# Kernel tuning notes

Hardware: AMD Instinct MI355X
Metric: run time of the kernel (lower is better)

## Reference

```python
import jax, jax.numpy as jnp
from jax import lax
import numpy as np

B, T, CIN, COUT = 64, 16384, 8, 8
N_A, N_B = 3, 3


def setup_inputs() -> dict:
    key = jax.random.key(0)
    k1, k2, k3, k4 = jax.random.split(key, 4)
    u = jax.random.normal(k1, (B, T, CIN), dtype=jnp.float32)
    x0 = jax.random.normal(k2, (B, N_A, COUT), dtype=jnp.float32)
    # Small AR coefficients so the IIR recursion is stable (sum |a_k| < 1).
    a_coeff = jax.random.uniform(k3, (N_A, COUT), dtype=jnp.float32,
                                 minval=-0.15, maxval=0.15)
    b_coeff = jax.random.normal(k4, (N_B + 1, CIN, COUT), dtype=jnp.float32)
    return {"u": u, "x0": x0, "a_coeff": a_coeff, "b_coeff": b_coeff}


def reference(u, x0, a_coeff, b_coeff):
    n_b = b_coeff.shape[0] - 1
    n_a = a_coeff.shape[0]
    # Causal FIR part: pad front of time axis, valid conv, channels_last.
    u_pad = jnp.pad(u, ((0, 0), (n_b, 0), (0, 0)))
    b_u = lax.conv_general_dilated(
        u_pad, b_coeff, window_strides=(1,), padding='VALID',
        dimension_numbers=('NWC', 'WIO', 'NWC'))  # [B, T, COUT]
    if n_a == 0:
        return b_u
    # Fold initial condition x0 into the first time step.
    first = b_u[:, 0, :] + jnp.einsum('to,bto->bo', jnp.flip(a_coeff, axis=0), x0)
    b_u = jnp.concatenate([first[:, None, :], b_u[:, 1:, :]], axis=1)
    # Stack n_a shifted copies (prepend tail of x0): [B, n_a, T, COUT]
    stacked = jnp.stack(
        [jnp.concatenate([x0[:, n_a - idx:, :], b_u[:, idx:, :]], axis=1)
         for idx in range(n_a)], axis=1)
    # Companion-style transition: a_ss[s, n, o] = a_coeff[n, o] if n >= s else 0.
    a_ss = jnp.stack(
        [jnp.pad(a_coeff[idx:, :], ((idx, 0), (0, 0))) for idx in range(n_a)],
        axis=0)  # [n_a, n_a, COUT]

    def a_apply(x, y):
        return jnp.einsum('sno,bnto->bsto', a_ss, x) + y

    y = lax.associative_scan(a_apply, stacked, axis=2)
    return y[:, 0, :, :]  # [B, T, COUT]
```

## Files before the change

kernel.cpp:

```cpp
#include <hip/hip_runtime.h>

#define T_SZ   16384
#define CIN    8
#define COUT   8
#define NPART  16
#define PART_T 1024
#define NCHUNK 32
#define CHT    32
#define GRID_BLOCKS (64 * NPART)
#define BAR_OFFSET_BYTES (1 << 17)

struct V3 { float x, y, z; };
__device__ __forceinline__ V3 mkv3(float a, float b, float c) { V3 r; r.x=a; r.y=b; r.z=c; return r; }
__device__ __forceinline__ V3 vadd3(V3 a, V3 b) { return mkv3(a.x+b.x, a.y+b.y, a.z+b.z); }
__device__ __forceinline__ V3 vfma3(V3 acc, float s, V3 w) {
  return mkv3(fmaf(s, w.x, acc.x), fmaf(s, w.y, acc.y), fmaf(s, w.z, acc.z));
}
__device__ __forceinline__ V3 aappf(float a0, float a1, float a2, V3 v) {
  float t2 = a2 * v.z;
  float t1 = fmaf(a1, v.y, t2);
  return mkv3(fmaf(a0, v.x, t1), t1, t2);
}
__device__ __forceinline__ V3 comb(float a0, float a1, float a2, V3 l, V3 r) {
  return vadd3(aappf(a0, a1, a2, l), r);
}

struct Row { float4 lo, hi; };
__device__ __forceinline__ Row ldrow(const float* p) {
  Row r; r.lo = *(const float4*)p; r.hi = *(const float4*)(p + 4); return r;
}
__device__ __forceinline__ Row zrow() { Row r; r.lo = make_float4(0.f,0.f,0.f,0.f); r.hi = r.lo; return r; }
__device__ __forceinline__ float rdot(const Row& r, const float* w) {
  float s = r.lo.x * w[0];
  s = fmaf(r.lo.y, w[1], s); s = fmaf(r.lo.z, w[2], s); s = fmaf(r.lo.w, w[3], s);
  s = fmaf(r.hi.x, w[4], s); s = fmaf(r.hi.y, w[5], s); s = fmaf(r.hi.z, w[6], s);
  s = fmaf(r.hi.w, w[7], s);
  return s;
}

struct Pre {
  float bv[CHT];
  V3 e0, e1, E5;
  float a0, a1, a2;
  int o, c, p, b, t0;
};

__device__ __forceinline__ void preamble(
    Pre& P, const float* __restrict__ u, const float* __restrict__ x0,
    const float* __restrict__ ac, const float* __restrict__ bc)
{
  const int j = threadIdx.x;
  P.o = j & 7;  P.c = j >> 3;
  P.p = blockIdx.x & 15;  P.b = blockIdx.x >> 4;
  const int o = P.o;
  P.a0 = ac[0*COUT + o];  P.a1 = ac[1*COUT + o];  P.a2 = ac[2*COUT + o];
  const float a0 = P.a0, a1 = P.a1, a2 = P.a2;

  float w0[8], w1[8], w2[8], w3[8];
#pragma unroll
  for (int i = 0; i < 8; ++i) {
    w0[i] = bc[(0*CIN + i)*COUT + o];
    w1[i] = bc[(1*CIN + i)*COUT + o];
    w2[i] = bc[(2*CIN + i)*COUT + o];
    w3[i] = bc[(3*CIN + i)*COUT + o];
  }

  const float* ub = u + (size_t)P.b * T_SZ * CIN;
  P.t0 = P.p * PART_T + P.c * CHT;
  const int t0 = P.t0;

  {
    Row ra, rb, rc;
    if (t0 == 0) { ra = zrow(); rb = zrow(); rc = zrow(); }
    else {
      ra = ldrow(ub + (size_t)(t0 - 3) * CIN);
      rb = ldrow(ub + (size_t)(t0 - 2) * CIN);
      rc = ldrow(ub + (size_t)(t0 - 1) * CIN);
    }
#pragma unroll
    for (int r = 0; r < CHT; ++r) {
      Row rd = ldrow(ub + (size_t)(t0 + r) * CIN);
      P.bv[r] = rdot(ra, w0) + rdot(rb, w1) + rdot(rc, w2) + rdot(rd, w3);
      ra = rb; rb = rc; rc = rd;
    }
  }

  P.e0 = mkv3(0,0,0);  P.e1 = mkv3(0,0,0);
  if (t0 == 0) {
    float x00 = x0[((size_t)P.b*3 + 0)*COUT + o];
    float x01 = x0[((size_t)P.b*3 + 1)*COUT + o];
    float x02 = x0[((size_t)P.b*3 + 2)*COUT + o];
    float first = P.bv[0] + a2*x00 + a1*x01 + a0*x02;
    P.e0 = mkv3(first, x02, x01);
    P.e1 = mkv3(P.bv[1], P.bv[1], x02);
  }

  V3 gt[6];
  gt[0] = mkv3(1.f,1.f,1.f);
#pragma unroll
  for (int k = 1; k <= 5; ++k) gt[k] = aappf(a0,a1,a2, gt[k-1]);
  V3 acc;
  if (t0 == 0) {
    V3 q0 = P.e0, q1 = P.e1;
#pragma unroll
    for (int k = 0; k < 5; ++k) q0 = aappf(a0,a1,a2, q0);
#pragma unroll
    for (int k = 0; k < 4; ++k) q1 = aappf(a0,a1,a2, q1);
    acc = vadd3(q0, q1);
#pragma unroll
    for (int r = 2; r < CHT; ++r) acc = vfma3(acc, P.bv[r], gt[5 - __popc(r)]);
  } else {
    acc = mkv3(0,0,0);
#pragma unroll
    for (int r = 0; r < CHT; ++r) acc = vfma3(acc, P.bv[r], gt[5 - __popc(r)]);
  }
  P.E5 = acc;
}

__global__ __launch_bounds__(256) void ldtf_p1(
    const float* __restrict__ u, const float* __restrict__ x0,
    const float* __restrict__ ac, const float* __restrict__ bc,
    float* __restrict__ ws)
{
  __shared__ V3 s_E5[NCHUNK*8];
  __shared__ V3 s_tr[30*8];

  Pre P;
  preamble(P, u, x0, ac, bc);
  const int j = threadIdx.x, o = P.o;
  const float a0 = P.a0, a1 = P.a1, a2 = P.a2;

  s_E5[P.c*8 + o] = P.E5;
  __syncthreads();
  if (j < 128) { int i = j >> 3; s_tr[i*8+o]      = comb(a0,a1,a2, s_E5[(2*i)*8+o],    s_E5[(2*i+1)*8+o]); }
  __syncthreads();
  if (j < 64)  { int i = j >> 3; s_tr[(16+i)*8+o] = comb(a0,a1,a2, s_tr[(2*i)*8+o],    s_tr[(2*i+1)*8+o]); }
  __syncthreads();
  if (j < 32)  { int i = j >> 3; s_tr[(24+i)*8+o] = comb(a0,a1,a2, s_tr[(16+2*i)*8+o], s_tr[(16+2*i+1)*8+o]); }
  __syncthreads();
  if (j < 16)  { int i = j >> 3; s_tr[(28+i)*8+o] = comb(a0,a1,a2, s_tr[(24+2*i)*8+o], s_tr[(24+2*i+1)*8+o]); }
  __syncthreads();
  if (j < 8) {
    V3 rt = comb(a0,a1,a2, s_tr[28*8+o], s_tr[29*8+o]);
    float* wp = ws + ((size_t)(P.b*NPART + P.p)*8 + o)*3;
    wp[0] = rt.x; wp[1] = rt.y; wp[2] = rt.z;
  }
}

#define POOL_FLOATS 8448

__global__ __launch_bounds__(256) void ldtf_p2(
    const float* __restrict__ u, const float* __restrict__ x0,
    const float* __restrict__ ac, const float* __restrict__ bc,
    float* __restrict__ out, const float* __restrict__ ws)
{
  __shared__ __align__(16) float s_pool[POOL_FLOATS];
  V3* s_E5 = (V3*)s_pool;
  V3* s_tr = (V3*)s_pool + 256;
  V3* s_mt = (V3*)s_pool + 496;
  float* s_out = s_pool;

  Pre P;
  preamble(P, u, x0, ac, bc);
  const int j = threadIdx.x, o = P.o, c = P.c, p = P.p, b = P.b;
  const float a0 = P.a0, a1 = P.a1, a2 = P.a2;

  s_E5[c*8 + o] = P.E5;
  if (j < 128) {
    int c2 = j >> 3;
    const float* wp = ws + ((size_t)(b*NPART + c2)*8 + o)*3;
    s_mt[c2*8+o] = mkv3(wp[0], wp[1], wp[2]);
  }
  __syncthreads();

  if (j < 128) { int i = j >> 3; s_tr[i*8+o]      = comb(a0,a1,a2, s_E5[(2*i)*8+o],    s_E5[(2*i+1)*8+o]); }
  else         { int i = (j-128) >> 3; if (i < 8) s_mt[(16+i)*8+o] = comb(a0,a1,a2, s_mt[(2*i)*8+o], s_mt[(2*i+1)*8+o]); }
  __syncthreads();
  if (j < 64)  { int i = j >> 3; s_tr[(16+i)*8+o] = comb(a0,a1,a2, s_tr[(2*i)*8+o],    s_tr[(2*i+1)*8+o]); }
  else if (j >= 128) { int i = (j-128) >> 3; if (i < 4) s_mt[(24+i)*8+o] = comb(a0,a1,a2, s_mt[(16+2*i)*8+o], s_mt[(16+2*i+1)*8+o]); }
  __syncthreads();
  if (j < 32)  { int i = j >> 3; s_tr[(24+i)*8+o] = comb(a0,a1,a2, s_tr[(16+2*i)*8+o], s_tr[(16+2*i+1)*8+o]); }
  else if (j >= 128) { int i = (j-128) >> 3; if (i < 2) s_mt[(28+i)*8+o] = comb(a0,a1,a2, s_mt[(24+2*i)*8+o], s_mt[(24+2*i+1)*8+o]); }
  __syncthreads();
  if (j < 16)  { int i = j >> 3; s_tr[(28+i)*8+o] = comb(a0,a1,a2, s_tr[(24+2*i)*8+o], s_tr[(24+2*i+1)*8+o]); }
  __syncthreads();

  V3 sig = mkv3(0,0,0);
  if ((p >> 3) & 1) sig = comb(a0,a1,a2, sig, s_mt[(28 + (p>>3) - 1)*8 + o]);
  if ((p >> 2) & 1) sig = comb(a0,a1,a2, sig, s_mt[(24 + (p>>2) - 1)*8 + o]);
  if ((p >> 1) & 1) sig = comb(a0,a1,a2, sig, s_mt[(16 + (p>>1) - 1)*8 + o]);
  if (p & 1)        sig = comb(a0,a1,a2, sig, s_mt[(p - 1)*8 + o]);
  if ((c >> 4) & 1) sig = comb(a0,a1,a2, sig, s_tr[(28 + (c>>4) - 1)*8 + o]);
  if ((c >> 3) & 1) sig = comb(a0,a1,a2, sig, s_tr[(24 + (c>>3) - 1)*8 + o]);
  if ((c >> 2) & 1) sig = comb(a0,a1,a2, sig, s_tr[(16 + (c>>2) - 1)*8 + o]);
  if ((c >> 1) & 1) sig = comb(a0,a1,a2, sig, s_tr[((c>>1) - 1)*8 + o]);
  if (c & 1)        sig = comb(a0,a1,a2, sig, s_E5[(c - 1)*8 + o]);

  V3 tau;
  {
    int q = p + 1;
    if (q == 16) tau = comb(a0,a1,a2, s_mt[28*8+o], s_mt[29*8+o]);
    else {
      tau = mkv3(0,0,0);
      if ((q >> 3) & 1) tau = comb(a0,a1,a2, tau, s_mt[(28 + (q>>3) - 1)*8 + o]);
      if ((q >> 2) & 1) tau = comb(a0,a1,a2, tau, s_mt[(24 + (q>>2) - 1)*8 + o]);
      if ((q >> 1) & 1) tau = comb(a0,a1,a2, tau, s_mt[(16 + (q>>1) - 1)*8 + o]);
      if (q & 1)        tau = comb(a0,a1,a2, tau, s_mt[(q - 1)*8 + o]);
    }
  }
  __syncthreads();

  if (c >= 1) s_out[(c - 1)*264 + 31*8 + o] = sig.x;
  if (c == NCHUNK - 1) s_out[31*264 + 31*8 + o] = tau.x;

  {
    V3 st[5];
#pragma unroll
    for (int r = 0; r < CHT - 1; ++r) {
      V3 v = mkv3(P.bv[r], P.bv[r], P.bv[r]);
      if (P.t0 == 0) { if (r == 0) v = P.e0; if (r == 1) v = P.e1; }
      if (r & 1)          v = comb(a0,a1,a2, st[0], v);
      if ((r & 3) == 3)   v = comb(a0,a1,a2, st[1], v);
      if ((r & 7) == 7)   v = comb(a0,a1,a2, st[2], v);
      if ((r & 15) == 15) v = comb(a0,a1,a2, st[3], v);
      const int lvl = (r & 1) ? (((r & 3) == 3) ? (((r & 7) == 7) ? (((r & 15) == 15) ? 4 : 3) : 2) : 1) : 0;
      st[lvl] = v;
      const int i = r + 1;
      V3 acc = sig;
      if (i & 16) acc = comb(a0,a1,a2, acc, st[4]);
      if (i & 8)  acc = comb(a0,a1,a2, acc, st[3]);
      if (i & 4)  acc = comb(a0,a1,a2, acc, st[2]);
      if (i & 2)  acc = comb(a0,a1,a2, acc, st[1]);
      if (i & 1)  acc = comb(a0,a1,a2, acc, st[0]);
      s_out[c*264 + r*8 + o] = acc.x;
    }
  }
  __syncthreads();

  float* og = out + ((size_t)b * T_SZ + (size_t)p * PART_T) * COUT;
#pragma unroll
  for (int it = 0; it < 8; ++it) {
    int f = (it * 256 + j) * 4;
    float4 v = *(const float4*)&s_out[(f >> 8) * 264 + (f & 255)];
    *(float4*)&og[f] = v;
  }
}

__global__ __launch_bounds__(256, 4) void ldtf_fused1024(
    const float* __restrict__ u, const float* __restrict__ x0,
    const float* __restrict__ ac, const float* __restrict__ bc,
    float* __restrict__ out, float* __restrict__ ws,
    unsigned int* __restrict__ bar)
{
  __shared__ V3 s_lf[NCHUNK*8];
  __shared__ V3 s_tr[30*8];
  __shared__ V3 s_mt[30*8];

  const int j = threadIdx.x;
  const int o = j & 7, c = j >> 3;
  const int p = blockIdx.x & 15, b = blockIdx.x >> 4;

  const float a0 = ac[0*COUT + o], a1 = ac[1*COUT + o], a2 = ac[2*COUT + o];

  const float* ub = u + (size_t)b * T_SZ * CIN;
  const int t0 = p * PART_T + c * CHT;
  const bool z0 = (t0 == 0);

  float bv[CHT];
  {
    float w0[8], w1[8], w2[8], w3[8];
#pragma unroll
    for (int i = 0; i < 8; ++i) {
      w0[i] = bc[(0*CIN + i)*COUT + o];
      w1[i] = bc[(1*CIN + i)*COUT + o];
      w2[i] = bc[(2*CIN + i)*COUT + o];
      w3[i] = bc[(3*CIN + i)*COUT + o];
    }
    Row ra, rb, rc;
    if (z0) { ra = zrow(); rb = zrow(); rc = zrow(); }
    else {
      ra = ldrow(ub + (size_t)(t0 - 3) * CIN);
      rb = ldrow(ub + (size_t)(t0 - 2) * CIN);
      rc = ldrow(ub + (size_t)(t0 - 1) * CIN);
    }
#pragma unroll
    for (int r = 0; r < CHT; ++r) {
      Row rd = ldrow(ub + (size_t)(t0 + r) * CIN);
      bv[r] = rdot(ra, w0) + rdot(rb, w1) + rdot(rc, w2) + rdot(rd, w3);
      ra = rb; rb = rc; rc = rd;
    }
  }

  V3 e0 = mkv3(0,0,0), e1 = mkv3(0,0,0);
  if (z0) {
    float x00 = x0[((size_t)b*3 + 0)*COUT + o];
    float x01 = x0[((size_t)b*3 + 1)*COUT + o];
    float x02 = x0[((size_t)b*3 + 2)*COUT + o];
    float first = bv[0] + a2*x00 + a1*x01 + a0*x02;
    e0 = mkv3(first, x02, x01);
    e1 = mkv3(bv[1], bv[1], x02);
  }

  {
    V3 gt[6];
    gt[0] = mkv3(1.f,1.f,1.f);
#pragma unroll
    for (int k = 1; k <= 5; ++k) gt[k] = aappf(a0,a1,a2, gt[k-1]);
    V3 acc;
    if (z0) {
      V3 q0 = e0, q1 = e1;
#pragma unroll
      for (int k = 0; k < 5; ++k) q0 = aappf(a0,a1,a2, q0);
#pragma unroll
      for (int k = 0; k < 4; ++k) q1 = aappf(a0,a1,a2, q1);
      acc = vadd3(q0, q1);
#pragma unroll
      for (int r = 2; r < CHT; ++r) acc = vfma3(acc, bv[r], gt[5 - __popc(r)]);
    } else {
      acc = mkv3(0,0,0);
#pragma unroll
      for (int r = 0; r < CHT; ++r) acc = vfma3(acc, bv[r], gt[5 - __popc(r)]);
    }
    s_lf[c*8 + o] = acc;
  }
  __syncthreads();

  if (j < 128) { int i = j >> 3; s_tr[i*8+o]      = comb(a0,a1,a2, s_lf[(2*i)*8+o],    s_lf[(2*i+1)*8+o]); }
  __syncthreads();
  if (j < 64)  { int i = j >> 3; s_tr[(16+i)*8+o] = comb(a0,a1,a2, s_tr[(2*i)*8+o],    s_tr[(2*i+1)*8+o]); }
  __syncthreads();
  if (j < 32)  { int i = j >> 3; s_tr[(24+i)*8+o] = comb(a0,a1,a2, s_tr[(16+2*i)*8+o], s_tr[(16+2*i+1)*8+o]); }
  __syncthreads();
  if (j < 16)  { int i = j >> 3; s_tr[(28+i)*8+o] = comb(a0,a1,a2, s_tr[(24+2*i)*8+o], s_tr[(24+2*i+1)*8+o]); }
  __syncthreads();
  if (j < 8) {
    V3 rt = comb(a0,a1,a2, s_tr[28*8+o], s_tr[29*8+o]);
    float* wp = ws + ((size_t)(b*NPART + p)*8 + o)*3;
    __hip_atomic_store(wp + 0, rt.x, __ATOMIC_RELAXED, __HIP_MEMORY_SCOPE_AGENT);
    __hip_atomic_store(wp + 1, rt.y, __ATOMIC_RELAXED, __HIP_MEMORY_SCOPE_AGENT);
    __hip_atomic_store(wp + 2, rt.z, __ATOMIC_RELAXED, __HIP_MEMORY_SCOPE_AGENT);
  }

  __syncthreads();
  if (j == 0) {
    __threadfence();
    atomicAdd(bar, 1u);
    while (__hip_atomic_load(bar, __ATOMIC_ACQUIRE, __HIP_MEMORY_SCOPE_AGENT)
           < (unsigned)GRID_BLOCKS) {
      __builtin_amdgcn_s_sleep(2);
    }
  }
  __syncthreads();
  __threadfence();

  if (j < 128) {
    int c2 = j >> 3;
    const float* wp = ws + ((size_t)(b*NPART + c2)*8 + o)*3;
    float rx = __hip_atomic_load(wp + 0, __ATOMIC_RELAXED, __HIP_MEMORY_SCOPE_AGENT);
    float ry = __hip_atomic_load(wp + 1, __ATOMIC_RELAXED, __HIP_MEMORY_SCOPE_AGENT);
    float rz = __hip_atomic_load(wp + 2, __ATOMIC_RELAXED, __HIP_MEMORY_SCOPE_AGENT);
    s_mt[c2*8 + o] = mkv3(rx, ry, rz);
  }
  __syncthreads();
  if (j < 64) { int i = j >> 3; s_mt[(16+i)*8+o] = comb(a0,a1,a2, s_mt[(2*i)*8+o],    s_mt[(2*i+1)*8+o]); }
  __syncthreads();
  if (j < 32) { int i = j >> 3; s_mt[(24+i)*8+o] = comb(a0,a1,a2, s_mt[(16+2*i)*8+o], s_mt[(16+2*i+1)*8+o]); }
  __syncthreads();
  if (j < 16) { int i = j >> 3; s_mt[(28+i)*8+o] = comb(a0,a1,a2, s_mt[(24+2*i)*8+o], s_mt[(24+2*i+1)*8+o]); }
  __syncthreads();

  V3 sig = mkv3(0,0,0);
  if ((p >> 3) & 1) sig = comb(a0,a1,a2, sig, s_mt[(28 + (p>>3) - 1)*8 + o]);
  if ((p >> 2) & 1) sig = comb(a0,a1,a2, sig, s_mt[(24 + (p>>2) - 1)*8 + o]);
  if ((p >> 1) & 1) sig = comb(a0,a1,a2, sig, s_mt[(16 + (p>>1) - 1)*8 + o]);
  if (p & 1)        sig = comb(a0,a1,a2, sig, s_mt[(p - 1)*8 + o]);
  if ((c >> 4) & 1) sig = comb(a0,a1,a2, sig, s_tr[(28 + (c>>4) - 1)*8 + o]);
  if ((c >> 3) & 1) sig = comb(a0,a1,a2, sig, s_tr[(24 + (c>>3) - 1)*8 + o]);
  if ((c >> 2) & 1) sig = comb(a0,a1,a2, sig, s_tr[(16 + (c>>2) - 1)*8 + o]);
  if ((c >> 1) & 1) sig = comb(a0,a1,a2, sig, s_tr[((c>>1) - 1)*8 + o]);
  if (c & 1)        sig = comb(a0,a1,a2, sig, s_lf[(c - 1)*8 + o]);

  float* og = out + ((size_t)b * T_SZ + (size_t)t0) * COUT + o;

  if (c >= 1) *(og - 8) = sig.x;

  if (c == NCHUNK - 1) {
    V3 tau;
    int q = p + 1;
    if (q == 16) tau = comb(a0,a1,a2, s_mt[28*8+o], s_mt[29*8+o]);
    else {
      tau = mkv3(0,0,0);
      if ((q >> 3) & 1) tau = comb(a0,a1,a2, tau, s_mt[(28 + (q>>3) - 1)*8 + o]);
      if ((q >> 2) & 1) tau = comb(a0,a1,a2, tau, s_mt[(24 + (q>>2) - 1)*8 + o]);
      if ((q >> 1) & 1) tau = comb(a0,a1,a2, tau, s_mt[(16 + (q>>1) - 1)*8 + o]);
      if (q & 1)        tau = comb(a0,a1,a2, tau, s_mt[(q - 1)*8 + o]);
    }
    og[31*8] = tau.x;
  }

  {
    V3 st[5];
#pragma unroll
    for (int r = 0; r < CHT - 1; ++r) {
      V3 v = mkv3(bv[r], bv[r], bv[r]);
      if (z0) { if (r == 0) v = e0; if (r == 1) v = e1; }
      if (r & 1)          v = comb(a0,a1,a2, st[0], v);
      if ((r & 3) == 3)   v = comb(a0,a1,a2, st[1], v);
      if ((r & 7) == 7)   v = comb(a0,a1,a2, st[2], v);
      if ((r & 15) == 15) v = comb(a0,a1,a2, st[3], v);
      const int lvl = (r & 1) ? (((r & 3) == 3) ? (((r & 7) == 7) ? (((r & 15) == 15) ? 4 : 3) : 2) : 1) : 0;
      st[lvl] = v;
      const int i = r + 1;
      V3 acc = sig;
      if (i & 16) acc = comb(a0,a1,a2, acc, st[4]);
      if (i & 8)  acc = comb(a0,a1,a2, acc, st[3]);
      if (i & 4)  acc = comb(a0,a1,a2, acc, st[2]);
      if (i & 2)  acc = comb(a0,a1,a2, acc, st[1]);
      if (i & 1)  acc = comb(a0,a1,a2, acc, st[0]);
      og[r*8] = acc.x;
    }
  }
}

extern "C" void kernel_launch(void* const* d_in, const int* in_sizes, int n_in,
                              void* d_out, int out_size, void* d_ws, size_t ws_size,
                              hipStream_t stream) {
  const float* u  = (const float*)d_in[0];
  const float* x0 = (const float*)d_in[1];
  const float* ac = (const float*)d_in[2];
  const float* bc = (const float*)d_in[3];
  float* outp = (float*)d_out;
  float* wsp  = (float*)d_ws;
  (void)in_sizes; (void)n_in; (void)out_size;

  static int fused_ok = -1;
  if (fused_ok < 0) {
    int nb = 0, ncu = 0, dev = 0;
    hipGetDevice(&dev);
    hipDeviceProp_t prop;
    if (hipGetDeviceProperties(&prop, dev) == hipSuccess) ncu = prop.multiProcessorCount;
    if (hipOccupancyMaxActiveBlocksPerMultiprocessor(&nb, ldtf_fused1024, 256, 0) != hipSuccess) nb = 0;
    fused_ok = (nb > 0 && ncu > 0 && (long)nb * ncu >= GRID_BLOCKS &&
                ws_size >= (size_t)BAR_OFFSET_BYTES + 16) ? 1 : 0;
  }

  if (fused_ok == 1) {
    unsigned int* bar = (unsigned int*)((char*)d_ws + BAR_OFFSET_BYTES);
    hipMemsetAsync(bar, 0, sizeof(unsigned int), stream);
    ldtf_fused1024<<<dim3(GRID_BLOCKS), dim3(256), 0, stream>>>(u, x0, ac, bc, outp, wsp, bar);
  } else {
    ldtf_p1<<<dim3(GRID_BLOCKS), dim3(256), 0, stream>>>(u, x0, ac, bc, wsp);
    ldtf_p2<<<dim3(GRID_BLOCKS), dim3(256), 0, stream>>>(u, x0, ac, bc, outp, wsp);
  }
}
```

Measured before the change: 133.9 us.

## Replace grid-wide barrier with per-partition ready flags for lookback

The single atomic counter barrier that made every block wait for all 1024 blocks is replaced by one ready flag per (batch, partition). Each block publishes its partition total, sets its flag with release semantics, and then spins only on the flags of earlier partitions in the same batch. Entries for later partitions are zeroed so the existing tree prefix still works. The intent is to cut grid-wide barrier stalls and drop the co-residency occupancy check. The cost is that the minimum-blocks launch bound is removed, which may change register allocation, and progress now depends on lower-index blocks being scheduled first.

```diff
diff --git a/kernel.cpp b/kernel.cpp
--- a/kernel.cpp
+++ b/kernel.cpp
@@ -8,7 +8,7 @@
 #define NCHUNK 32
 #define CHT    32
 #define GRID_BLOCKS (64 * NPART)
-#define BAR_OFFSET_BYTES (1 << 17)
+#define FLAG_OFFSET_BYTES (1 << 17)
 
 struct V3 { float x, y, z; };
 __device__ __forceinline__ V3 mkv3(float a, float b, float c) { V3 r; r.x=a; r.y=b; r.z=c; return r; }
@@ -246,11 +246,11 @@
   }
 }
 
-__global__ __launch_bounds__(256, 4) void ldtf_fused1024(
+__global__ __launch_bounds__(256) void ldtf_dlb(
     const float* __restrict__ u, const float* __restrict__ x0,
     const float* __restrict__ ac, const float* __restrict__ bc,
     float* __restrict__ out, float* __restrict__ ws,
-    unsigned int* __restrict__ bar)
+    unsigned int* __restrict__ flags)
 {
   __shared__ V3 s_lf[NCHUNK*8];
   __shared__ V3 s_tr[30*8];
@@ -333,35 +333,38 @@
   __syncthreads();
   if (j < 16)  { int i = j >> 3; s_tr[(28+i)*8+o] = comb(a0,a1,a2, s_tr[(24+2*i)*8+o], s_tr[(24+2*i+1)*8+o]); }
   __syncthreads();
+
   if (j < 8) {
     V3 rt = comb(a0,a1,a2, s_tr[28*8+o], s_tr[29*8+o]);
+    s_mt[p*8 + o] = rt;
     float* wp = ws + ((size_t)(b*NPART + p)*8 + o)*3;
     __hip_atomic_store(wp + 0, rt.x, __ATOMIC_RELAXED, __HIP_MEMORY_SCOPE_AGENT);
     __hip_atomic_store(wp + 1, rt.y, __ATOMIC_RELAXED, __HIP_MEMORY_SCOPE_AGENT);
     __hip_atomic_store(wp + 2, rt.z, __ATOMIC_RELAXED, __HIP_MEMORY_SCOPE_AGENT);
   }
-
   __syncthreads();
   if (j == 0) {
-    __threadfence();
-    atomicAdd(bar, 1u);
-    while (__hip_atomic_load(bar, __ATOMIC_ACQUIRE, __HIP_MEMORY_SCOPE_AGENT)
-           < (unsigned)GRID_BLOCKS) {
-      __builtin_amdgcn_s_sleep(2);
-    }
-  }
-  __syncthreads();
-  __threadfence();
+    __hip_atomic_store(&flags[b*NPART + p], 1u, __ATOMIC_RELEASE, __HIP_MEMORY_SCOPE_AGENT);
+  }
 
   if (j < 128) {
-    int c2 = j >> 3;
-    const float* wp = ws + ((size_t)(b*NPART + c2)*8 + o)*3;
-    float rx = __hip_atomic_load(wp + 0, __ATOMIC_RELAXED, __HIP_MEMORY_SCOPE_AGENT);
-    float ry = __hip_atomic_load(wp + 1, __ATOMIC_RELAXED, __HIP_MEMORY_SCOPE_AGENT);
-    float rz = __hip_atomic_load(wp + 2, __ATOMIC_RELAXED, __HIP_MEMORY_SCOPE_AGENT);
-    s_mt[c2*8 + o] = mkv3(rx, ry, rz);
-  }
-  __syncthreads();
+    int q = j >> 3;
+    if (q < p) {
+      const unsigned int* fq = &flags[b*NPART + q];
+      while (__hip_atomic_load(fq, __ATOMIC_ACQUIRE, __HIP_MEMORY_SCOPE_AGENT) == 0u) {
+        __builtin_amdgcn_s_sleep(1);
+      }
+      const float* wp = ws + ((size_t)(b*NPART + q)*8 + o)*3;
+      float rx = __hip_atomic_load(wp + 0, __ATOMIC_RELAXED, __HIP_MEMORY_SCOPE_AGENT);
+      float ry = __hip_atomic_load(wp + 1, __ATOMIC_RELAXED, __HIP_MEMORY_SCOPE_AGENT);
+      float rz = __hip_atomic_load(wp + 2, __ATOMIC_RELAXED, __HIP_MEMORY_SCOPE_AGENT);
+      s_mt[q*8 + o] = mkv3(rx, ry, rz);
+    } else if (q > p) {
+      s_mt[q*8 + o] = mkv3(0.f, 0.f, 0.f);
+    }
+  }
+  __syncthreads();
+
   if (j < 64) { int i = j >> 3; s_mt[(16+i)*8+o] = comb(a0,a1,a2, s_mt[(2*i)*8+o],    s_mt[(2*i+1)*8+o]); }
   __syncthreads();
   if (j < 32) { int i = j >> 3; s_mt[(24+i)*8+o] = comb(a0,a1,a2, s_mt[(16+2*i)*8+o], s_mt[(16+2*i+1)*8+o]); }
@@ -433,21 +436,10 @@
   float* wsp  = (float*)d_ws;
   (void)in_sizes; (void)n_in; (void)out_size;
 
-  static int fused_ok = -1;
-  if (fused_ok < 0) {
-    int nb = 0, ncu = 0, dev = 0;
-    hipGetDevice(&dev);
-    hipDeviceProp_t prop;
-    if (hipGetDeviceProperties(&prop, dev) == hipSuccess) ncu = prop.multiProcessorCount;
-    if (hipOccupancyMaxActiveBlocksPerMultiprocessor(&nb, ldtf_fused1024, 256, 0) != hipSuccess) nb = 0;
-    fused_ok = (nb > 0 && ncu > 0 && (long)nb * ncu >= GRID_BLOCKS &&
-                ws_size >= (size_t)BAR_OFFSET_BYTES + 16) ? 1 : 0;
-  }
-
-  if (fused_ok == 1) {
-    unsigned int* bar = (unsigned int*)((char*)d_ws + BAR_OFFSET_BYTES);
-    hipMemsetAsync(bar, 0, sizeof(unsigned int), stream);
-    ldtf_fused1024<<<dim3(GRID_BLOCKS), dim3(256), 0, stream>>>(u, x0, ac, bc, outp, wsp, bar);
+  if (ws_size >= (size_t)FLAG_OFFSET_BYTES + GRID_BLOCKS * sizeof(unsigned int)) {
+    unsigned int* flg = (unsigned int*)((char*)d_ws + FLAG_OFFSET_BYTES);
+    hipMemsetAsync(flg, 0, GRID_BLOCKS * sizeof(unsigned int), stream);
+    ldtf_dlb<<<dim3(GRID_BLOCKS), dim3(256), 0, stream>>>(u, x0, ac, bc, outp, wsp, flg);
   } else {
     ldtf_p1<<<dim3(GRID_BLOCKS), dim3(256), 0, stream>>>(u, x0, ac, bc, wsp);
     ldtf_p2<<<dim3(GRID_BLOCKS), dim3(256), 0, stream>>>(u, x0, ac, bc, outp, wsp);
```

After: 134.9 us. No clear change (+0.8%).
